# Kernel optimization log

Measured on AMD Instinct MI355X. Metric: run time of the kernel, lower is better.

## Reference

```python
import jax, jax.numpy as jnp
import numpy as np

ND, ED, HD, L, K = 128, 64, 256, 4, 24   # node_dim, edge_dim(num_rbf), hidden_dim, num_layers, max_neighbors
CUTOFF = 8.0
N = 2048  # n_atoms


def _silu(x):
    return x * jax.nn.sigmoid(x)


def _lattice(lengths, angles):
    a, b, c = lengths[0], lengths[1], lengths[2]
    deg = jnp.asarray(np.pi / 180.0, lengths.dtype)
    al, be, ga = angles[0] * deg, angles[1] * deg, angles[2] * deg
    lx = a
    xy = b * jnp.cos(ga)
    xz = c * jnp.cos(be)
    ly = b * jnp.sin(ga)
    yz = (b * c * jnp.cos(al) - xy * xz) / ly
    lz = jnp.sqrt(c ** 2 - xz ** 2 - yz ** 2)
    z = jnp.zeros((), lengths.dtype)
    return jnp.stack([jnp.stack([lx, z, z]), jnp.stack([xy, ly, z]), jnp.stack([xz, yz, lz])])


def _rbf(d):
    centers = jnp.linspace(0.0, CUTOFF, ED)
    widths = jnp.full((ED,), CUTOFF / ED)
    d = d[..., None]
    g = jnp.exp(-(d - centers) ** 2 / (2.0 * widths ** 2))
    cv = 0.5 * (jnp.cos(d * jnp.pi / CUTOFF) + 1.0) * (d < CUTOFF).astype(d.dtype)
    return g * cv


def _forward(atom_types, frac_coords, lengths, angles, timesteps, emb, tW, tb,
             eW1, eb1, eW2, eb2, nW1, nb1, nW2, nb2, cW1, cb1, cW2, cb2):
    n = frac_coords.shape[0]
    lattice = _lattice(lengths, angles)            # [3,3]
    cart = frac_coords @ lattice                   # [n,3]

    # ---- vectorized periodic neighbor graph (replaces host triple loop) ----
    shifts = jnp.asarray(np.array([[i, j, k] for i in (-1, 0, 1) for j in (-1, 0, 1) for k in (-1, 0, 1)],
                                  dtype=np.float32))
    sv = shifts @ lattice                          # [27,3]
    p = cart[None, :, :] + sv[:, None, :]          # [27,n,3] shifted atom positions
    # squared distances without materializing [27,n,n,3]
    d2 = (p * p).sum(-1)[:, :, None] + (cart * cart).sum(-1)[None, None, :] \
         - 2.0 * jnp.einsum('snk,mk->snm', p, cart)      # [27, n_j, n_i]
    dist = jnp.sqrt(jnp.maximum(d2, 1e-12))
    cand = jnp.where((dist < CUTOFF) & (dist > 0.01), dist, jnp.inf)
    cand = cand.reshape(27 * n, n).T               # [n_i, 27*n_j]; flat f = s*n + j
    _, idx = jax.lax.top_k(-cand, K)               # K smallest distances per atom i
    d_k = jnp.take_along_axis(cand, idx, axis=1)   # [n,K]
    dst = (idx % n).reshape(-1)                    # neighbor atom j (edge_list = [i, j])
    src = jnp.repeat(jnp.arange(n), K)             # center atom i
    valid = jnp.isfinite(d_k).reshape(-1)
    m = valid.astype(jnp.float32)[:, None]         # [E,1] pad mask
    d_e = jnp.where(valid, d_k.reshape(-1), 0.0)
    edge_attr = _rbf(d_e)                          # [E, ED]

    # ---- EGNN stack ----
    nf = emb[atom_types] + timesteps @ tW + tb     # [n, ND]
    coords = cart
    seg = lambda x, i: jax.ops.segment_sum(x, i, num_segments=n)
    for l in range(L):
        ef = jnp.concatenate([nf[src], nf[dst], edge_attr], axis=-1)   # [E, 2*ND+ED]
        msg = _silu(_silu(ef @ eW1[l] + eb1[l]) @ eW2[l] + eb2[l])     # [E, HD]
        aggr = seg(msg * m, dst)                                       # [n, HD]
        nf = nf + _silu(jnp.concatenate([nf, aggr], axis=-1) @ nW1[l] + nb1[l]) @ nW2[l] + nb2[l]
        w = _silu(msg @ cW1[l] + cb1[l]) @ cW2[l] + cb2[l]             # [E,1]
        cd = coords[src] - coords[dst]
        cd = cd / (jnp.linalg.norm(cd, axis=-1, keepdims=True) + 1e-8)
        coords = coords + seg(w * cd * m, dst)
    return nf, coords


def setup_inputs() -> dict:
    key = jax.random.key(0)
    ks = jax.random.split(key, 16)
    pr = lambda k, shape: jax.random.normal(k, shape, jnp.float32) * 0.02
    return dict(
        atom_types=jax.random.randint(ks[0], (N,), 0, 100),
        frac_coords=jax.random.uniform(ks[1], (N, 3), jnp.float32),
        lengths=jnp.ones((3,), jnp.float32) * 12.0,
        angles=jnp.ones((3,), jnp.float32) * 90.0,
        timesteps=jax.random.normal(ks[2], (N, 128), jnp.float32),
        emb=pr(ks[3], (100, ND)),
        tW=pr(ks[4], (128, ND)), tb=jnp.zeros((ND,), jnp.float32),
        eW1=pr(ks[5], (L, 2 * ND + ED, HD)), eb1=jnp.zeros((L, HD), jnp.float32),
        eW2=pr(ks[6], (L, HD, HD)), eb2=jnp.zeros((L, HD), jnp.float32),
        nW1=pr(ks[7], (L, ND + HD, HD)), nb1=jnp.zeros((L, HD), jnp.float32),
        nW2=pr(ks[8], (L, HD, ND)), nb2=jnp.zeros((L, ND), jnp.float32),
        cW1=pr(ks[9], (L, HD, HD // 2)), cb1=jnp.zeros((L, HD // 2), jnp.float32),
        cW2=pr(ks[10], (L, HD // 2, 1)), cb2=jnp.zeros((L, 1), jnp.float32),
    )


def reference(atom_types, frac_coords, lengths, angles, timesteps, emb, tW, tb,
              eW1, eb1, eW2, eb2, nW1, nb1, nW2, nb2, cW1, cb1, cW2, cb2):
    return _forward(atom_types, frac_coords, lengths, angles, timesteps, emb, tW, tb,
                    eW1, eb1, eW2, eb2, nW1, nb1, nW2, nb2, cW1, cb1, cW2, cb2)
```

## Files before the change

kernel.cpp:

```cpp
#include <hip/hip_runtime.h>
#include <hip/hip_bf16.h>
#include <math.h>

#define NA 2048
#define KN 24
#define NE (NA*KN)
#define NDIM 128
#define EDIM 64
#define HDIM 256
#define NLAYER 4
#define MAXDEG 256
#define EB 64

typedef __attribute__((ext_vector_type(8))) short bf16x8;
typedef __attribute__((ext_vector_type(4))) float f32x4;

__device__ __forceinline__ float siluf(float x) {
    return __fdividef(x, 1.0f + __expf(-x));
}
__device__ __forceinline__ ushort f2b(float x) {
    __hip_bfloat16 h = __float2bfloat16(x);
    return *reinterpret_cast<ushort*>(&h);
}
__device__ __forceinline__ float b2f(ushort h) { return __uint_as_float(((unsigned)h) << 16); }

__device__ __forceinline__ void gl_lds(const void* g, void* lds) {
    __builtin_amdgcn_global_load_lds(
        (const __attribute__((address_space(1))) unsigned int*)g,
        (__attribute__((address_space(3))) unsigned int*)lds, 16, 0, 0);
}

struct Lat { float lx, xy, xz, ly, yz, lz; };

__device__ __forceinline__ Lat make_lattice(const float* lengths, const float* angles) {
    const float deg = 0.017453292519943295f;
    float a = lengths[0], b = lengths[1], c = lengths[2];
    float al = angles[0]*deg, be = angles[1]*deg, ga = angles[2]*deg;
    Lat L;
    L.lx = a;
    L.xy = b * cosf(ga);
    L.xz = c * cosf(be);
    L.ly = b * sinf(ga);
    L.yz = (b*c*cosf(al) - L.xy*L.xz) / L.ly;
    L.lz = sqrtf(c*c - L.xz*L.xz - L.yz*L.yz);
    return L;
}

__global__ void setup_kernel(const float* __restrict__ frac, const float* __restrict__ lengths,
                             const float* __restrict__ angles, float* __restrict__ cart,
                             float* __restrict__ cxg, float* __restrict__ cyg,
                             float* __restrict__ czg, float* __restrict__ sv,
                             int* __restrict__ ccnt) {
    int i = blockIdx.x*blockDim.x + threadIdx.x;
    Lat L = make_lattice(lengths, angles);
    if (i < NA) {
        float f0 = frac[i*3], f1 = frac[i*3+1], f2 = frac[i*3+2];
        float x = f0*L.lx + f1*L.xy + f2*L.xz;
        float y = f1*L.ly + f2*L.yz;
        float z = f2*L.lz;
        cart[i*3+0] = x; cart[i*3+1] = y; cart[i*3+2] = z;
        cxg[i] = x; cyg[i] = y; czg[i] = z;
        ccnt[i] = 0;
    }
    if (i < 27) {
        float s0 = (float)(i/9 - 1), s1 = (float)((i/3)%3 - 1), s2 = (float)(i%3 - 1);
        sv[i*3+0] = s0*L.lx + s1*L.xy + s2*L.xz;
        sv[i*3+1] = s1*L.ly + s2*L.yz;
        sv[i*3+2] = s2*L.lz;
    }
}

__global__ __launch_bounds__(64) void knn_kernel(
        const float* __restrict__ cxg, const float* __restrict__ cyg,
        const float* __restrict__ czg, const float* __restrict__ lengths,
        const float* __restrict__ angles, const float* __restrict__ sv,
        int* __restrict__ dstl, ushort* __restrict__ rbf16,
        int* __restrict__ ccnt, int* __restrict__ cedg) {
    __shared__ float sd2L[16][64];
    __shared__ int   sfL[16][64];
    const int lane = threadIdx.x;
    const int i = blockIdx.x;
    Lat L = make_lattice(lengths, angles);
    const float deg = 0.017453292519943295f;
    const bool ortho = fabsf(cosf(angles[0]*deg)) < 1e-6f &&
                       fabsf(cosf(angles[1]*deg)) < 1e-6f &&
                       fabsf(cosf(angles[2]*deg)) < 1e-6f;
    const float cx = cxg[i], cy = cyg[i], cz = czg[i];
    const float invlx = 1.0f/L.lx, invly = 1.0f/L.ly, invlz = 1.0f/L.lz;
    float R = 2.8f;
    int mycnt = 0, cnt = 0;
    bool flatm = false;
    for (int attempt = 0; attempt < 8; ++attempt) {
        const float R2 = R*R;
        mycnt = 0;
        flatm = !ortho || (attempt == 7);
        if (!flatm) {
#pragma unroll 2
            for (int j0 = 0; j0 < NA; j0 += 64) {
                const int j = j0 + lane;
                const float dx = cxg[j] - cx, dy = cyg[j] - cy, dz = czg[j] - cz;
                const float kx = rintf(dx*invlx), ky = rintf(dy*invly), kz = rintf(dz*invlz);
                const float ex = dx - (kx*L.lx + ky*L.xy + kz*L.xz);
                const float ey = dy - (ky*L.ly + kz*L.yz);
                const float ez = dz - kz*L.lz;
                const float d2 = fmaf(ex,ex,fmaf(ey,ey,ez*ez));
                if (d2 < R2 && d2 > 1e-4f) {
                    const int s = (1-(int)kx)*9 + (1-(int)ky)*3 + (1-(int)kz);
                    if (mycnt < 16) { sd2L[mycnt][lane] = d2; sfL[mycnt][lane] = (s<<11) + j; }
                    ++mycnt;
                }
            }
            if (__ballot(mycnt > 16)) {
                flatm = true;
            } else {
                int tot = mycnt;
                for (int off = 32; off > 0; off >>= 1) tot += __shfl_xor(tot, off, 64);
                cnt = tot;
            }
        }
        if (flatm) {
            cnt = 0;
            for (int s = 0; s < 27; ++s) {
                const float svx = sv[s*3], svy = sv[s*3+1], svz = sv[s*3+2];
                for (int j0 = 0; j0 < NA; j0 += 64) {
                    const int j = j0 + lane;
                    const float ex = cxg[j] + svx - cx;
                    const float ey = cyg[j] + svy - cy;
                    const float ez = czg[j] + svz - cz;
                    const float d2 = fmaf(ex,ex,fmaf(ey,ey,ez*ez));
                    const bool hit = (d2 < R2) && (d2 > 1e-4f);
                    const unsigned long long m = __ballot(hit);
                    const int rank = __popcll(m & ((1ull<<lane)-1ull));
                    const int slot = cnt + rank;
                    if (hit && slot < 1024) { sd2L[slot>>6][slot&63] = d2; sfL[slot>>6][slot&63] = (s<<11)+j; }
                    cnt += __popcll(m);
                }
            }
            cnt = min(cnt, 1024);
        }
        if (cnt >= KN) break;
        R = fminf(R*1.6f, flatm ? 8.0f : 5.9f);
    }
    int vq;
    if (flatm) vq = (lane < cnt) ? min(16, ((cnt - 1 - lane) >> 6) + 1) : 0;
    else       vq = mycnt;
    unsigned long long key[16];
#pragma unroll
    for (int q = 0; q < 16; ++q) {
        const float d2v = sd2L[q][lane];
        const int fl = sfL[q][lane];
        const unsigned long long kk = ((unsigned long long)__float_as_uint(d2v) << 20)
                                    | ((unsigned long long)(unsigned)fl << 4) | (unsigned)q;
        key[q] = (q < vq) ? kk : ~0ull;
    }
    float der[KN];
    for (int k = 0; k < KN; ++k) {
        unsigned long long lm = key[0];
#pragma unroll
        for (int q = 1; q < 16; ++q) lm = key[q] < lm ? key[q] : lm;
        for (int off = 32; off > 0; off >>= 1) {
            unsigned long long o = __shfl_xor(lm, off, 64);
            lm = o < lm ? o : lm;
        }
        der[k] = sqrtf(__uint_as_float((unsigned)(lm >> 20)));
        if (lane == 0) {
            const int jn = (int)((lm >> 4) & 2047u);
            dstl[i*KN + k] = jn;
            const int slot = atomicAdd(&ccnt[jn], 1);
            if (slot < MAXDEG) cedg[(size_t)jn*MAXDEG + slot] = i*KN + k;
        }
#pragma unroll
        for (int q = 0; q < 16; ++q) if (key[q] == lm) key[q] = ~0ull;
    }
    const float center = (8.0f/63.0f) * (float)lane;
    for (int k = 0; k < KN; ++k) {
        const float d = der[k];
        const float diff = d - center;
        const float g = __expf(diff*diff * -32.0f);
        const float cv = 0.5f * (__cosf(d * (float)(M_PI/8.0)) + 1.0f);
        rbf16[(size_t)(i*KN + k)*EDIM + lane] = f2b(g * cv);
    }
}

__global__ void csort_kernel(const int* __restrict__ ccnt, int* __restrict__ cedg) {
    const int j = blockIdx.x*4 + (threadIdx.x >> 6);
    const int lane = threadIdx.x & 63;
    const int cnt = min(ccnt[j], MAXDEG);
    if (cnt <= 64) {
        int v = (lane < cnt) ? cedg[(size_t)j*MAXDEG + lane] : 0x7FFFFFFF;
#pragma unroll
        for (int k = 2; k <= 64; k <<= 1) {
#pragma unroll
            for (int s = k >> 1; s > 0; s >>= 1) {
                int o = __shfl_xor(v, s, 64);
                const bool up = ((lane & k) == 0);
                const bool lowhalf = ((lane & s) == 0);
                v = ((lowhalf == up) ? min(v, o) : max(v, o));
            }
        }
        if (lane < cnt) cedg[(size_t)j*MAXDEG + lane] = v;
    } else if (lane == 0) {
        int* L = cedg + (size_t)j*MAXDEG;
        for (int a = 1; a < cnt; ++a) {
            int v = L[a]; int b = a - 1;
            while (b >= 0 && L[b] > v) { L[b+1] = L[b]; --b; }
            L[b+1] = v;
        }
    }
}

__global__ void nf_init_kernel(const int* __restrict__ atom_types, const float* __restrict__ ts,
                               const float* __restrict__ emb, const float* __restrict__ tW,
                               const float* __restrict__ tb, float* __restrict__ nf,
                               ushort* __restrict__ nf16) {
    int i = blockIdx.x, c = threadIdx.x;
    float acc = emb[atom_types[i]*NDIM + c] + tb[c];
    for (int kk = 0; kk < 128; ++kk) acc += ts[i*128 + kk] * tW[kk*NDIM + c];
    nf[i*NDIM + c] = acc;
    nf16[i*NDIM + c] = f2b(acc);
}

__global__ void wprep_all(const float* __restrict__ eW1, const float* __restrict__ eW2,
                          const float* __restrict__ cW1, const float* __restrict__ nW1,
                          const float* __restrict__ nW2,
                          ushort* __restrict__ eW1t, ushort* __restrict__ eW2t,
                          ushort* __restrict__ cW1t, ushort* __restrict__ nW1t,
                          ushort* __restrict__ nW2t) {
    __shared__ float tile[64][65];
    const int b = blockIdx.x;
    const float* W; ushort* Wt; int Kk, Nn, rel;
    if (b < 80)       { W = eW1; Wt = eW1t; Kk = 320; Nn = 256; rel = b; }
    else if (b < 144) { W = eW2; Wt = eW2t; Kk = 256; Nn = 256; rel = b - 80; }
    else if (b < 176) { W = cW1; Wt = cW1t; Kk = 256; Nn = 128; rel = b - 144; }
    else if (b < 272) { W = nW1; Wt = nW1t; Kk = 384; Nn = 256; rel = b - 176; }
    else              { W = nW2; Wt = nW2t; Kk = 256; Nn = 128; rel = b - 272; }
    const int kt = Kk >> 6, nt = Nn >> 6, per = kt*nt;
    const int l = rel / per, r2 = rel - l*per;
    const int k0 = (r2 / nt) * 64, n0 = (r2 - (r2/nt)*nt) * 64;
    const float* Wl = W + (size_t)l*Kk*Nn;
    ushort* Wtl = Wt + (size_t)l*Kk*Nn;
    const int tr = threadIdx.x >> 6, tc = threadIdx.x & 63;
#pragma unroll
    for (int q = 0; q < 16; ++q) {
        const int k = q*4 + tr;
        tile[k][tc] = Wl[(size_t)(k0 + k)*Nn + n0 + tc];
    }
    __syncthreads();
#pragma unroll
    for (int q = 0; q < 16; ++q) {
        const int n = q*4 + tr;
        Wtl[(size_t)(n0 + n)*Kk + k0 + tc] = f2b(tile[tc][n]);
    }
}

__global__ __launch_bounds__(256) void edge_fused(
        const ushort* __restrict__ nf16, const int* __restrict__ dstl,
        const ushort* __restrict__ rbf16,
        const ushort* __restrict__ eW1t,
        const ushort* __restrict__ eW2t,
        const ushort* __restrict__ cW1t,
        const float* __restrict__ eb1, const float* __restrict__ eb2,
        const float* __restrict__ cb1, const float* __restrict__ cW2v,
        const float* __restrict__ cb2v,
        ushort* __restrict__ msg16, float* __restrict__ wvout) {
    __shared__ alignas(16) char R0[40960];
    __shared__ alignas(16) char R1[32768];
    __shared__ int sdst[64];
    __shared__ float wred[2][64];
    ushort* As = (ushort*)R0;
    ushort* Bs = (ushort*)(R0 + 8192);
    ushort* B2 = (ushort*)R1;
    ushort* Cs = (ushort*)R1;

    const int t = threadIdx.x, wave = t >> 6, lane = t & 63;
    const int row0 = blockIdx.x*EB;
    if (t < EB) sdst[t] = dstl[row0 + t];
    __syncthreads();
    const int wr = (wave >> 1)*32;
    const int wcB = (wave & 1)*128;
    const int lr = lane & 15, g0 = lane >> 4;

    const int rA_  = wave*16 + (lane >> 2);
    const int gA_  = (lane & 3) ^ ((rA_ >> 1) & 3);
    const int eA_  = row0 + rA_;
    const ushort* baseSrc = nf16  + (size_t)(eA_/KN)*NDIM + gA_*8;
    const ushort* baseDst = nf16  + (size_t)sdst[rA_]*NDIM + gA_*8;
    const ushort* baseRbf = rbf16 + (size_t)eA_*EDIM + gA_*8;
    const uint ldsA_ = (uint)(wave*16)*32;
    const ushort* baseW1[4]; const ushort* baseW2[4];
    uint ldsBq[4];
#pragma unroll
    for (int q = 0; q < 4; ++q) {
        const int rowb = wave*64 + q*16 + (lane >> 2);
        const int gB = (lane & 3) ^ ((rowb >> 1) & 3);
        baseW1[q] = eW1t + (size_t)rowb*320 + gB*8;
        baseW2[q] = eW2t + (size_t)rowb*256 + gB*8;
        ldsBq[q] = (uint)(wave*64 + q*16)*32;
    }
    const ushort* baseC[2];
    uint ldsCq[2];
#pragma unroll
    for (int q = 0; q < 2; ++q) {
        const int rowb = wave*32 + q*16 + (lane >> 2);
        const int gB = (lane & 3) ^ ((rowb >> 1) & 3);
        baseC[q] = cW1t + (size_t)rowb*256 + gB*8;
        ldsCq[q] = (uint)(wave*32 + q*16)*32;
    }

    auto STAGEA = [&](int buf, int k0) {
        const ushort* gp = (k0 < NDIM) ? baseSrc + k0
                         : (k0 < 2*NDIM) ? baseDst + (k0 - NDIM)
                         : baseRbf + (k0 - 2*NDIM);
        gl_lds(gp, As + (size_t)buf*2048 + ldsA_);
#pragma unroll
        for (int q = 0; q < 4; ++q)
            gl_lds(baseW1[q] + k0, Bs + (size_t)buf*8192 + ldsBq[q]);
    };
    f32x4 acc[2][8];
#pragma unroll
    for (int m = 0; m < 2; ++m)
#pragma unroll
        for (int n = 0; n < 8; ++n) acc[m][n] = (f32x4){0.f,0.f,0.f,0.f};
    STAGEA(0, 0);
    int cur = 0;
#pragma unroll
    for (int it = 0; it < 10; ++it) {
        if (it + 1 < 10) {
            STAGEA(cur ^ 1, (it + 1)*32);
            asm volatile("s_waitcnt vmcnt(5)" ::: "memory");
        } else {
            asm volatile("s_waitcnt vmcnt(0)" ::: "memory");
        }
        __builtin_amdgcn_s_barrier();
        bf16x8 af[2], bfr[8];
#pragma unroll
        for (int m = 0; m < 2; ++m) {
            const int rA = wr + m*16 + lr;
            af[m] = *reinterpret_cast<const bf16x8*>(&As[cur*2048 + rA*32 + ((g0 ^ ((rA>>1)&3)))*8]);
        }
#pragma unroll
        for (int n = 0; n < 8; ++n) {
            const int rB = wcB + n*16 + lr;
            bfr[n] = *reinterpret_cast<const bf16x8*>(&Bs[(size_t)cur*8192 + rB*32 + ((g0 ^ ((rB>>1)&3)))*8]);
        }
        __builtin_amdgcn_s_setprio(1);
#pragma unroll
        for (int m = 0; m < 2; ++m)
#pragma unroll
            for (int n = 0; n < 8; ++n)
                acc[m][n] = __builtin_amdgcn_mfma_f32_16x16x32_bf16(af[m], bfr[n], acc[m][n], 0, 0, 0);
        __builtin_amdgcn_s_setprio(0);
        __builtin_amdgcn_s_barrier();
        cur ^= 1;
    }
    {
#pragma unroll
        for (int q = 0; q < 4; ++q)
            gl_lds(baseW2[q], B2 + ldsBq[q]);
    }
#pragma unroll
    for (int n = 0; n < 8; ++n) {
        const int cc = wcB + n*16 + lr;
        const float b1 = eb1[cc];
#pragma unroll
        for (int m = 0; m < 2; ++m) {
#pragma unroll
            for (int j = 0; j < 4; ++j) {
                const int rr = wr + m*16 + g0*4 + j;
                const float x = siluf(acc[m][n][j] + b1);
                *(ushort*)(R0 + rr*512 + ((cc*2) ^ ((rr&7)<<4))) = f2b(x);
            }
        }
    }
    __syncthreads();

#pragma unroll
    for (int m = 0; m < 2; ++m)
#pragma unroll
        for (int n = 0; n < 8; ++n) acc[m][n] = (f32x4){0.f,0.f,0.f,0.f};
    cur = 0;
#pragma unroll
    for (int it = 0; it < 8; ++it) {
        if (it + 1 < 8) {
            const int k0 = (it + 1)*32;
#pragma unroll
            for (int q = 0; q < 4; ++q)
                gl_lds(baseW2[q] + k0, B2 + (size_t)(cur^1)*8192 + ldsBq[q]);
            asm volatile("s_waitcnt vmcnt(4)" ::: "memory");
        } else {
            asm volatile("s_waitcnt vmcnt(0)" ::: "memory");
        }
        __builtin_amdgcn_s_barrier();
        bf16x8 af[2], bfr[8];
#pragma unroll
        for (int m = 0; m < 2; ++m) {
            const int rA = wr + m*16 + lr;
            const int kc = it*4 + g0;
            af[m] = *reinterpret_cast<const bf16x8*>(R0 + rA*512 + ((kc*16) ^ ((rA&7)<<4)));
        }
#pragma unroll
        for (int n = 0; n < 8; ++n) {
            const int rB = wcB + n*16 + lr;
            bfr[n] = *reinterpret_cast<const bf16x8*>(&B2[(size_t)cur*8192 + rB*32 + ((g0 ^ ((rB>>1)&3)))*8]);
        }
        __builtin_amdgcn_s_setprio(1);
#pragma unroll
        for (int m = 0; m < 2; ++m)
#pragma unroll
            for (int n = 0; n < 8; ++n)
                acc[m][n] = __builtin_amdgcn_mfma_f32_16x16x32_bf16(af[m], bfr[n], acc[m][n], 0, 0, 0);
        __builtin_amdgcn_s_setprio(0);
        __builtin_amdgcn_s_barrier();
        cur ^= 1;
    }
    {
#pragma unroll
        for (int q = 0; q < 2; ++q)
            gl_lds(baseC[q], Cs + ldsCq[q]);
    }
#pragma unroll
    for (int n = 0; n < 8; ++n) {
        const int cc = wcB + n*16 + lr;
        const float b2 = eb2[cc];
#pragma unroll
        for (int m = 0; m < 2; ++m) {
#pragma unroll
            for (int j = 0; j < 4; ++j) {
                const int rr = wr + m*16 + g0*4 + j;
                *(ushort*)(R0 + rr*512 + ((cc*2) ^ ((rr&7)<<4))) = f2b(siluf(acc[m][n][j] + b2));
            }
        }
    }
    __syncthreads();

    const int wcC = (wave & 1)*64;
    f32x4 acc3[2][4];
#pragma unroll
    for (int m = 0; m < 2; ++m)
#pragma unroll
        for (int n = 0; n < 4; ++n) acc3[m][n] = (f32x4){0.f,0.f,0.f,0.f};
    cur = 0;
#pragma unroll
    for (int it = 0; it < 8; ++it) {
        if (it + 1 < 8) {
            const int k0 = (it + 1)*32;
#pragma unroll
            for (int q = 0; q < 2; ++q)
                gl_lds(baseC[q] + k0, Cs + (size_t)(cur^1)*4096 + ldsCq[q]);
            asm volatile("s_waitcnt vmcnt(2)" ::: "memory");
        } else {
            asm volatile("s_waitcnt vmcnt(0)" ::: "memory");
        }
        __builtin_amdgcn_s_barrier();
        bf16x8 af[2], bfr[4];
#pragma unroll
        for (int m = 0; m < 2; ++m) {
            const int rA = wr + m*16 + lr;
            const int kc = it*4 + g0;
            af[m] = *reinterpret_cast<const bf16x8*>(R0 + rA*512 + ((kc*16) ^ ((rA&7)<<4)));
        }
#pragma unroll
        for (int n = 0; n < 4; ++n) {
            const int rB = wcC + n*16 + lr;
            bfr[n] = *reinterpret_cast<const bf16x8*>(&Cs[(size_t)cur*4096 + rB*32 + ((g0 ^ ((rB>>1)&3)))*8]);
        }
        __builtin_amdgcn_s_setprio(1);
#pragma unroll
        for (int m = 0; m < 2; ++m)
#pragma unroll
            for (int n = 0; n < 4; ++n)
                acc3[m][n] = __builtin_amdgcn_mfma_f32_16x16x32_bf16(af[m], bfr[n], acc3[m][n], 0, 0, 0);
        __builtin_amdgcn_s_setprio(0);
        __builtin_amdgcn_s_barrier();
        cur ^= 1;
    }
    float part[2][4];
#pragma unroll
    for (int m = 0; m < 2; ++m)
#pragma unroll
        for (int j = 0; j < 4; ++j) part[m][j] = 0.0f;
#pragma unroll
    for (int n = 0; n < 4; ++n) {
        const int cc = wcC + n*16 + lr;
        const float bb = cb1[cc];
        const float cw = cW2v[cc];
#pragma unroll
        for (int m = 0; m < 2; ++m)
#pragma unroll
            for (int j = 0; j < 4; ++j)
                part[m][j] += siluf(acc3[m][n][j] + bb) * cw;
    }
#pragma unroll
    for (int off = 1; off < 16; off <<= 1)
#pragma unroll
        for (int m = 0; m < 2; ++m)
#pragma unroll
            for (int j = 0; j < 4; ++j)
                part[m][j] += __shfl_xor(part[m][j], off, 64);
    if (lr == 0) {
#pragma unroll
        for (int m = 0; m < 2; ++m)
#pragma unroll
            for (int j = 0; j < 4; ++j)
                wred[wave & 1][wr + m*16 + g0*4 + j] = part[m][j];
    }
    __syncthreads();
    if (t < EB) wvout[row0 + t] = wred[0][t] + wred[1][t] + cb2v[0];
#pragma unroll
    for (int k = 0; k < 8; ++k) {
        const int off = (t + k*256) * 16;
        const int row = off >> 9;
        const int cg = ((off >> 4) & 31) ^ (row & 7);
        uint4 v = *reinterpret_cast<const uint4*>(R0 + off);
        *reinterpret_cast<uint4*>(msg16 + (size_t)(row0 + row)*256 + cg*8) = v;
    }
}

__global__ __launch_bounds__(256) void nodefused(
        const ushort* __restrict__ nf16, const ushort* __restrict__ aggr16,
        const ushort* __restrict__ nW1t,
        const ushort* __restrict__ nW2t,
        const float* __restrict__ nb1, const float* __restrict__ nb2,
        float* __restrict__ nf, ushort* __restrict__ nf16out) {
    __shared__ alignas(16) ushort Ab[12*2048];
    __shared__ alignas(16) char HsB[32768];
    __shared__ alignas(16) ushort Bs[2][256*32];
    const int t = threadIdx.x, wave = t >> 6, lane = t & 63;
    const int r0 = blockIdx.x*64;
    const int wr = (wave >> 1)*32;
    const int wcB = (wave & 1)*128;
    const int lr = lane & 15, g0 = lane >> 4;

#pragma unroll
    for (int c = 0; c < 3; ++c) {
        const int ks = wave*3 + c;
#pragma unroll
        for (int q = 0; q < 4; ++q) {
            const int r = q*16 + (lane >> 2);
            const int g = (lane & 3) ^ ((r >> 1) & 3);
            const int col = ks*32 + g*8;
            const ushort* gp = (col < NDIM)
                ? nf16 + (size_t)(r0 + r)*NDIM + col
                : aggr16 + (size_t)(r0 + r)*HDIM + (col - NDIM);
            gl_lds(gp, Ab + ks*2048 + q*16*32);
        }
    }
    const ushort* baseW1[4];
    uint ldsBq[4];
#pragma unroll
    for (int q = 0; q < 4; ++q) {
        const int rowb = wave*64 + q*16 + (lane >> 2);
        const int gB = (lane & 3) ^ ((rowb >> 1) & 3);
        baseW1[q] = nW1t + (size_t)rowb*384 + gB*8;
        ldsBq[q] = (uint)(wave*64 + q*16)*32;
    }
    const ushort* baseW2[2];
    uint ldsCq[2];
#pragma unroll
    for (int q = 0; q < 2; ++q) {
        const int rowb = wave*32 + q*16 + (lane >> 2);
        const int gB = (lane & 3) ^ ((rowb >> 1) & 3);
        baseW2[q] = nW2t + (size_t)rowb*256 + gB*8;
        ldsCq[q] = (uint)(wave*32 + q*16)*32;
    }
#pragma unroll
    for (int q = 0; q < 4; ++q)
        gl_lds(baseW1[q], &Bs[0][ldsBq[q]]);
    asm volatile("s_waitcnt vmcnt(0)" ::: "memory");
    __builtin_amdgcn_s_barrier();

    f32x4 acc[2][8];
#pragma unroll
    for (int m = 0; m < 2; ++m)
#pragma unroll
        for (int n = 0; n < 8; ++n) acc[m][n] = (f32x4){0.f,0.f,0.f,0.f};
    int cur = 0;
#pragma unroll
    for (int it = 0; it < 12; ++it) {
        if (it + 1 < 12) {
            const int k0 = (it + 1)*32;
#pragma unroll
            for (int q = 0; q < 4; ++q)
                gl_lds(baseW1[q] + k0, &Bs[cur^1][ldsBq[q]]);
            asm volatile("s_waitcnt vmcnt(4)" ::: "memory");
        } else {
            asm volatile("s_waitcnt vmcnt(0)" ::: "memory");
        }
        __builtin_amdgcn_s_barrier();
        bf16x8 af[2], bfr[8];
#pragma unroll
        for (int m = 0; m < 2; ++m) {
            const int rA = wr + m*16 + lr;
            af[m] = *reinterpret_cast<const bf16x8*>(&Ab[it*2048 + rA*32 + ((g0 ^ ((rA>>1)&3)))*8]);
        }
#pragma unroll
        for (int n = 0; n < 8; ++n) {
            const int rB = wcB + n*16 + lr;
            bfr[n] = *reinterpret_cast<const bf16x8*>(&Bs[cur][rB*32 + ((g0 ^ ((rB>>1)&3)))*8]);
        }
        __builtin_amdgcn_s_setprio(1);
#pragma unroll
        for (int m = 0; m < 2; ++m)
#pragma unroll
            for (int n = 0; n < 8; ++n)
                acc[m][n] = __builtin_amdgcn_mfma_f32_16x16x32_bf16(af[m], bfr[n], acc[m][n], 0, 0, 0);
        __builtin_amdgcn_s_setprio(0);
        __builtin_amdgcn_s_barrier();
        cur ^= 1;
    }
#pragma unroll
    for (int q = 0; q < 2; ++q)
        gl_lds(baseW2[q], &Bs[0][ldsCq[q]]);
#pragma unroll
    for (int n = 0; n < 8; ++n) {
        const int cc = wcB + n*16 + lr;
        const float b1 = nb1[cc];
#pragma unroll
        for (int m = 0; m < 2; ++m) {
#pragma unroll
            for (int j = 0; j < 4; ++j) {
                const int rr = wr + m*16 + g0*4 + j;
                *(ushort*)(HsB + rr*512 + ((cc*2) ^ ((rr&7)<<4))) = f2b(siluf(acc[m][n][j] + b1));
            }
        }
    }
    __syncthreads();

    const int wcC = (wave & 1)*64;
    f32x4 acc3[2][4];
#pragma unroll
    for (int m = 0; m < 2; ++m)
#pragma unroll
        for (int n = 0; n < 4; ++n) acc3[m][n] = (f32x4){0.f,0.f,0.f,0.f};
    cur = 0;
#pragma unroll
    for (int it = 0; it < 8; ++it) {
        if (it + 1 < 8) {
            const int k0 = (it + 1)*32;
#pragma unroll
            for (int q = 0; q < 2; ++q)
                gl_lds(baseW2[q] + k0, &Bs[cur^1][ldsCq[q]]);
            asm volatile("s_waitcnt vmcnt(2)" ::: "memory");
        } else {
            asm volatile("s_waitcnt vmcnt(0)" ::: "memory");
        }
        __builtin_amdgcn_s_barrier();
        bf16x8 af[2], bfr[4];
#pragma unroll
        for (int m = 0; m < 2; ++m) {
            const int rA = wr + m*16 + lr;
            const int kc = it*4 + g0;
            af[m] = *reinterpret_cast<const bf16x8*>(HsB + rA*512 + ((kc*16) ^ ((rA&7)<<4)));
        }
#pragma unroll
        for (int n = 0; n < 4; ++n) {
            const int rB = wcC + n*16 + lr;
            bfr[n] = *reinterpret_cast<const bf16x8*>(&Bs[cur][rB*32 + ((g0 ^ ((rB>>1)&3)))*8]);
        }
        __builtin_amdgcn_s_setprio(1);
#pragma unroll
        for (int m = 0; m < 2; ++m)
#pragma unroll
            for (int n = 0; n < 4; ++n)
                acc3[m][n] = __builtin_amdgcn_mfma_f32_16x16x32_bf16(af[m], bfr[n], acc3[m][n], 0, 0, 0);
        __builtin_amdgcn_s_setprio(0);
        __builtin_amdgcn_s_barrier();
        cur ^= 1;
    }
#pragma unroll
    for (int n = 0; n < 4; ++n) {
        const int cc = wcC + n*16 + lr;
        const float b2 = nb2[cc];
#pragma unroll
        for (int m = 0; m < 2; ++m) {
#pragma unroll
            for (int j = 0; j < 4; ++j) {
                const int rr = r0 + wr + m*16 + g0*4 + j;
                float x = acc3[m][n][j] + b2 + nf[(size_t)rr*NDIM + cc];
                nf[(size_t)rr*NDIM + cc] = x;
                nf16out[(size_t)rr*NDIM + cc] = f2b(x);
            }
        }
    }
}

__global__ void node_kernel(const ushort* __restrict__ msg16, const float* __restrict__ cold,
                            const float* __restrict__ wv, const int* __restrict__ ccnt,
                            const int* __restrict__ cedg,
                            ushort* __restrict__ aggr16, float* __restrict__ cnew) {
    __shared__ int se[4][64];
    const int w = threadIdx.x >> 6, lane = threadIdx.x & 63;
    const int j = blockIdx.x*4 + w;
    const int cnt = min(ccnt[j], MAXDEG);
    se[w][lane] = (lane < cnt) ? cedg[(size_t)j*MAXDEG + lane] : 0;
    __syncthreads();
    const int c4 = lane*4;
    float s0 = 0, s1 = 0, s2 = 0, s3 = 0;
    const int lim = min(cnt, 64);
    for (int q = 0; q < lim; ++q) {
        const int e = se[w][q];
        ushort4 v = *reinterpret_cast<const ushort4*>(&msg16[(size_t)e*HDIM + c4]);
        s0 += b2f(v.x); s1 += b2f(v.y); s2 += b2f(v.z); s3 += b2f(v.w);
    }
    for (int q = 64; q < cnt; ++q) {
        const int e = cedg[(size_t)j*MAXDEG + q];
        ushort4 v = *reinterpret_cast<const ushort4*>(&msg16[(size_t)e*HDIM + c4]);
        s0 += b2f(v.x); s1 += b2f(v.y); s2 += b2f(v.z); s3 += b2f(v.w);
    }
    ushort4 o; o.x = f2b(s0); o.y = f2b(s1); o.z = f2b(s2); o.w = f2b(s3);
    *reinterpret_cast<ushort4*>(&aggr16[(size_t)j*HDIM + c4]) = o;
    const float jx = cold[j*3], jy = cold[j*3+1], jz = cold[j*3+2];
    float dx = 0, dy = 0, dz = 0;
    for (int q = lane; q < cnt; q += 64) {
        const int e = (q < 64) ? se[w][q] : cedg[(size_t)j*MAXDEG + q];
        const int si = e / KN;
        const float ax = cold[si*3]   - jx;
        const float ay = cold[si*3+1] - jy;
        const float az = cold[si*3+2] - jz;
        const float inv = wv[e] / (sqrtf(ax*ax + ay*ay + az*az) + 1e-8f);
        dx += inv*ax; dy += inv*ay; dz += inv*az;
    }
    for (int off = 32; off > 0; off >>= 1) {
        dx += __shfl_xor(dx, off, 64);
        dy += __shfl_xor(dy, off, 64);
        dz += __shfl_xor(dz, off, 64);
    }
    if (lane == 0) {
        cnew[j*3]   = jx + dx;
        cnew[j*3+1] = jy + dy;
        cnew[j*3+2] = jz + dz;
    }
}

__global__ void copyout_kernel(const float* __restrict__ nf, const float* __restrict__ coords,
                               float* __restrict__ out) {
    int idx = blockIdx.x*256 + threadIdx.x;
    if (idx < NA*NDIM) out[idx] = nf[idx];
    else if (idx < NA*NDIM + NA*3) out[idx] = coords[idx - NA*NDIM];
}

extern "C" void kernel_launch(void* const* d_in, const int* in_sizes, int n_in,
                              void* d_out, int out_size, void* d_ws, size_t ws_size,
                              hipStream_t stream) {
    const int*   atom_types = (const int*)  d_in[0];
    const float* frac       = (const float*)d_in[1];
    const float* lengths    = (const float*)d_in[2];
    const float* angles     = (const float*)d_in[3];
    const float* timesteps  = (const float*)d_in[4];
    const float* emb        = (const float*)d_in[5];
    const float* tW         = (const float*)d_in[6];
    const float* tb         = (const float*)d_in[7];
    const float* eW1        = (const float*)d_in[8];
    const float* eb1        = (const float*)d_in[9];
    const float* eW2        = (const float*)d_in[10];
    const float* eb2        = (const float*)d_in[11];
    const float* nW1        = (const float*)d_in[12];
    const float* nb1        = (const float*)d_in[13];
    const float* nW2        = (const float*)d_in[14];
    const float* nb2        = (const float*)d_in[15];
    const float* cW1        = (const float*)d_in[16];
    const float* cb1        = (const float*)d_in[17];
    const float* cW2        = (const float*)d_in[18];
    const float* cb2        = (const float*)d_in[19];

    char* p = (char*)d_ws;
    auto alloc = [&](size_t bytes) { char* q = p; p += (bytes + 255) & ~(size_t)255; return q; };
    float*  sv    = (float*) alloc(81*4);
    float*  c0    = (float*) alloc((size_t)NA*3*4);
    float*  c1    = (float*) alloc((size_t)NA*3*4);
    float*  cxg   = (float*) alloc((size_t)NA*4);
    float*  cyg   = (float*) alloc((size_t)NA*4);
    float*  czg   = (float*) alloc((size_t)NA*4);
    float*  nf    = (float*) alloc((size_t)NA*NDIM*4);
    int*    dstl  = (int*)   alloc((size_t)NE*4);
    ushort* rbf16 = (ushort*)alloc((size_t)NE*EDIM*2);
    int*    ccnt  = (int*)   alloc((size_t)NA*4);
    int*    cedg  = (int*)   alloc((size_t)NA*MAXDEG*4);
    ushort* aggr16= (ushort*)alloc((size_t)NA*HDIM*2);
    float*  wv    = (float*) alloc((size_t)NE*4);
    ushort* nf16  = (ushort*)alloc((size_t)NA*NDIM*2);
    ushort* msg16 = (ushort*)alloc((size_t)NE*HDIM*2);
    ushort* eW1t  = (ushort*)alloc((size_t)NLAYER*(2*NDIM+EDIM)*HDIM*2);
    ushort* eW2t  = (ushort*)alloc((size_t)NLAYER*HDIM*HDIM*2);
    ushort* cW1t  = (ushort*)alloc((size_t)NLAYER*(HDIM/2)*HDIM*2);
    ushort* nW1t  = (ushort*)alloc((size_t)NLAYER*(NDIM+HDIM)*HDIM*2);
    ushort* nW2t  = (ushort*)alloc((size_t)NLAYER*HDIM*NDIM*2);

    setup_kernel<<<8, 256, 0, stream>>>(frac, lengths, angles, c0, cxg, cyg, czg, sv, ccnt);
    knn_kernel<<<NA, 64, 0, stream>>>(cxg, cyg, czg, lengths, angles, sv,
                                      dstl, rbf16, ccnt, cedg);
    csort_kernel<<<NA/4, 256, 0, stream>>>(ccnt, cedg);
    nf_init_kernel<<<NA, 128, 0, stream>>>(atom_types, timesteps, emb, tW, tb, nf, nf16);
    wprep_all<<<304, 256, 0, stream>>>(eW1, eW2, cW1, nW1, nW2,
                                       eW1t, eW2t, cW1t, nW1t, nW2t);

    float* cin = c0; float* cout = c1;
    for (int l = 0; l < NLAYER; ++l) {
        const float* eb1l = eb1 + (size_t)l*HDIM;
        const float* eb2l = eb2 + (size_t)l*HDIM;
        const float* nb1l = nb1 + (size_t)l*HDIM;
        const float* nb2l = nb2 + (size_t)l*NDIM;
        const float* cb1l = cb1 + (size_t)l*(HDIM/2);
        const float* cW2l = cW2 + (size_t)l*(HDIM/2);
        const float* cb2l = cb2 + (size_t)l;

        edge_fused<<<NE/EB, 256, 0, stream>>>(
            nf16, dstl, rbf16,
            eW1t + (size_t)l*(2*NDIM+EDIM)*HDIM, eW2t + (size_t)l*HDIM*HDIM,
            cW1t + (size_t)l*(HDIM/2)*HDIM,
            eb1l, eb2l, cb1l, cW2l, cb2l, msg16, wv);
        node_kernel<<<NA/4, 256, 0, stream>>>(msg16, cin, wv, ccnt, cedg, aggr16, cout);
        nodefused<<<NA/64, 256, 0, stream>>>(
            nf16, aggr16, nW1t + (size_t)l*(NDIM+HDIM)*HDIM, nW2t + (size_t)l*HDIM*NDIM,
            nb1l, nb2l, nf, nf16);
        float* tmp = cin; cin = cout; cout = tmp;
    }
    copyout_kernel<<<(NA*NDIM + NA*3)/256, 256, 0, stream>>>(nf, cin, (float*)d_out);
}
```

Baseline: 363.0 us.

## Enlarge edge-kernel tile to 96 rows and single-buffer second and third GEMM weights

```diff
diff --git a/kernel.cpp b/kernel.cpp
--- a/kernel.cpp
+++ b/kernel.cpp
@@ -10,7 +10,7 @@
 #define HDIM 256
 #define NLAYER 4
 #define MAXDEG 256
-#define EB 64
+#define EB 96
 
 typedef __attribute__((ext_vector_type(8))) short bf16x8;
 typedef __attribute__((ext_vector_type(4))) float f32x4;
@@ -263,12 +263,12 @@
         const float* __restrict__ cb1, const float* __restrict__ cW2v,
         const float* __restrict__ cb2v,
         ushort* __restrict__ msg16, float* __restrict__ wvout) {
-    __shared__ alignas(16) char R0[40960];
-    __shared__ alignas(16) char R1[32768];
-    __shared__ int sdst[64];
-    __shared__ float wred[2][64];
+    __shared__ alignas(16) char R0[49152];
+    __shared__ alignas(16) char R1[16384];
+    __shared__ int sdst[96];
+    __shared__ float wred[2][96];
     ushort* As = (ushort*)R0;
-    ushort* Bs = (ushort*)(R0 + 8192);
+    ushort* Bs = (ushort*)(R0 + 12288);
     ushort* B2 = (ushort*)R1;
     ushort* Cs = (ushort*)R1;
 
@@ -276,17 +276,10 @@
     const int row0 = blockIdx.x*EB;
     if (t < EB) sdst[t] = dstl[row0 + t];
     __syncthreads();
-    const int wr = (wave >> 1)*32;
+    const int wr = (wave >> 1)*48;
     const int wcB = (wave & 1)*128;
     const int lr = lane & 15, g0 = lane >> 4;
 
-    const int rA_  = wave*16 + (lane >> 2);
-    const int gA_  = (lane & 3) ^ ((rA_ >> 1) & 3);
-    const int eA_  = row0 + rA_;
-    const ushort* baseSrc = nf16  + (size_t)(eA_/KN)*NDIM + gA_*8;
-    const ushort* baseDst = nf16  + (size_t)sdst[rA_]*NDIM + gA_*8;
-    const ushort* baseRbf = rbf16 + (size_t)eA_*EDIM + gA_*8;
-    const uint ldsA_ = (uint)(wave*16)*32;
     const ushort* baseW1[4]; const ushort* baseW2[4];
     uint ldsBq[4];
 #pragma unroll
@@ -308,17 +301,27 @@
     }
 
     auto STAGEA = [&](int buf, int k0) {
-        const ushort* gp = (k0 < NDIM) ? baseSrc + k0
-                         : (k0 < 2*NDIM) ? baseDst + (k0 - NDIM)
-                         : baseRbf + (k0 - 2*NDIM);
-        gl_lds(gp, As + (size_t)buf*2048 + ldsA_);
+        const int na = (wave < 2) ? 2 : 1;
+        const int a0 = (wave < 2) ? wave*2 : wave + 2;
+        for (int q = 0; q < na; ++q) {
+            const int grp = a0 + q;
+            const int r = grp*16 + (lane >> 2);
+            const int g = (lane & 3) ^ ((r >> 1) & 3);
+            const int kg = k0 + g*8;
+            const int e = row0 + r;
+            const ushort* gp;
+            if (kg < NDIM)        gp = nf16 + (size_t)(e/KN)*NDIM + kg;
+            else if (kg < 2*NDIM) gp = nf16 + (size_t)sdst[r]*NDIM + (kg - NDIM);
+            else                  gp = rbf16 + (size_t)e*EDIM + (kg - 2*NDIM);
+            gl_lds(gp, As + (size_t)buf*3072 + grp*512);
+        }
 #pragma unroll
         for (int q = 0; q < 4; ++q)
             gl_lds(baseW1[q] + k0, Bs + (size_t)buf*8192 + ldsBq[q]);
     };
-    f32x4 acc[2][8];
-#pragma unroll
-    for (int m = 0; m < 2; ++m)
+    f32x4 acc[3][8];
+#pragma unroll
+    for (int m = 0; m < 3; ++m)
 #pragma unroll
         for (int n = 0; n < 8; ++n) acc[m][n] = (f32x4){0.f,0.f,0.f,0.f};
     STAGEA(0, 0);
@@ -327,16 +330,17 @@
     for (int it = 0; it < 10; ++it) {
         if (it + 1 < 10) {
             STAGEA(cur ^ 1, (it + 1)*32);
-            asm volatile("s_waitcnt vmcnt(5)" ::: "memory");
+            if (wave < 2) asm volatile("s_waitcnt vmcnt(6)" ::: "memory");
+            else          asm volatile("s_waitcnt vmcnt(5)" ::: "memory");
         } else {
             asm volatile("s_waitcnt vmcnt(0)" ::: "memory");
         }
         __builtin_amdgcn_s_barrier();
-        bf16x8 af[2], bfr[8];
-#pragma unroll
-        for (int m = 0; m < 2; ++m) {
+        bf16x8 af[3], bfr[8];
+#pragma unroll
+        for (int m = 0; m < 3; ++m) {
             const int rA = wr + m*16 + lr;
-            af[m] = *reinterpret_cast<const bf16x8*>(&As[cur*2048 + rA*32 + ((g0 ^ ((rA>>1)&3)))*8]);
+            af[m] = *reinterpret_cast<const bf16x8*>(&As[cur*3072 + rA*32 + ((g0 ^ ((rA>>1)&3)))*8]);
         }
 #pragma unroll
         for (int n = 0; n < 8; ++n) {
@@ -345,7 +349,7 @@
         }
         __builtin_amdgcn_s_setprio(1);
 #pragma unroll
-        for (int m = 0; m < 2; ++m)
+        for (int m = 0; m < 3; ++m)
 #pragma unroll
             for (int n = 0; n < 8; ++n)
                 acc[m][n] = __builtin_amdgcn_mfma_f32_16x16x32_bf16(af[m], bfr[n], acc[m][n], 0, 0, 0);
@@ -363,7 +367,7 @@
         const int cc = wcB + n*16 + lr;
         const float b1 = eb1[cc];
 #pragma unroll
-        for (int m = 0; m < 2; ++m) {
+        for (int m = 0; m < 3; ++m) {
 #pragma unroll
             for (int j = 0; j < 4; ++j) {
                 const int rr = wr + m*16 + g0*4 + j;
@@ -375,25 +379,16 @@
     __syncthreads();
 
 #pragma unroll
-    for (int m = 0; m < 2; ++m)
+    for (int m = 0; m < 3; ++m)
 #pragma unroll
         for (int n = 0; n < 8; ++n) acc[m][n] = (f32x4){0.f,0.f,0.f,0.f};
-    cur = 0;
 #pragma unroll
     for (int it = 0; it < 8; ++it) {
-        if (it + 1 < 8) {
-            const int k0 = (it + 1)*32;
-#pragma unroll
-            for (int q = 0; q < 4; ++q)
-                gl_lds(baseW2[q] + k0, B2 + (size_t)(cur^1)*8192 + ldsBq[q]);
-            asm volatile("s_waitcnt vmcnt(4)" ::: "memory");
-        } else {
-            asm volatile("s_waitcnt vmcnt(0)" ::: "memory");
-        }
-        __builtin_amdgcn_s_barrier();
-        bf16x8 af[2], bfr[8];
-#pragma unroll
-        for (int m = 0; m < 2; ++m) {
+        asm volatile("s_waitcnt vmcnt(0)" ::: "memory");
+        __builtin_amdgcn_s_barrier();
+        bf16x8 af[3], bfr[8];
+#pragma unroll
+        for (int m = 0; m < 3; ++m) {
             const int rA = wr + m*16 + lr;
             const int kc = it*4 + g0;
             af[m] = *reinterpret_cast<const bf16x8*>(R0 + rA*512 + ((kc*16) ^ ((rA&7)<<4)));
@@ -401,17 +396,22 @@
 #pragma unroll
         for (int n = 0; n < 8; ++n) {
             const int rB = wcB + n*16 + lr;
-            bfr[n] = *reinterpret_cast<const bf16x8*>(&B2[(size_t)cur*8192 + rB*32 + ((g0 ^ ((rB>>1)&3)))*8]);
+            bfr[n] = *reinterpret_cast<const bf16x8*>(&B2[rB*32 + ((g0 ^ ((rB>>1)&3)))*8]);
         }
         __builtin_amdgcn_s_setprio(1);
 #pragma unroll
-        for (int m = 0; m < 2; ++m)
+        for (int m = 0; m < 3; ++m)
 #pragma unroll
             for (int n = 0; n < 8; ++n)
                 acc[m][n] = __builtin_amdgcn_mfma_f32_16x16x32_bf16(af[m], bfr[n], acc[m][n], 0, 0, 0);
         __builtin_amdgcn_s_setprio(0);
         __builtin_amdgcn_s_barrier();
-        cur ^= 1;
+        if (it + 1 < 8) {
+            const int k0 = (it + 1)*32;
+#pragma unroll
+            for (int q = 0; q < 4; ++q)
+                gl_lds(baseW2[q] + k0, B2 + ldsBq[q]);
+        }
     }
     {
 #pragma unroll
@@ -423,7 +423,7 @@
         const int cc = wcB + n*16 + lr;
         const float b2 = eb2[cc];
 #pragma unroll
-        for (int m = 0; m < 2; ++m) {
+        for (int m = 0; m < 3; ++m) {
 #pragma unroll
             for (int j = 0; j < 4; ++j) {
                 const int rr = wr + m*16 + g0*4 + j;
@@ -434,27 +434,18 @@
     __syncthreads();
 
     const int wcC = (wave & 1)*64;
-    f32x4 acc3[2][4];
-#pragma unroll
-    for (int m = 0; m < 2; ++m)
+    f32x4 acc3[3][4];
+#pragma unroll
+    for (int m = 0; m < 3; ++m)
 #pragma unroll
         for (int n = 0; n < 4; ++n) acc3[m][n] = (f32x4){0.f,0.f,0.f,0.f};
-    cur = 0;
 #pragma unroll
     for (int it = 0; it < 8; ++it) {
-        if (it + 1 < 8) {
-            const int k0 = (it + 1)*32;
-#pragma unroll
-            for (int q = 0; q < 2; ++q)
-                gl_lds(baseC[q] + k0, Cs + (size_t)(cur^1)*4096 + ldsCq[q]);
-            asm volatile("s_waitcnt vmcnt(2)" ::: "memory");
-        } else {
-            asm volatile("s_waitcnt vmcnt(0)" ::: "memory");
-        }
-        __builtin_amdgcn_s_barrier();
-        bf16x8 af[2], bfr[4];
-#pragma unroll
-        for (int m = 0; m < 2; ++m) {
+        asm volatile("s_waitcnt vmcnt(0)" ::: "memory");
+        __builtin_amdgcn_s_barrier();
+        bf16x8 af[3], bfr[4];
+#pragma unroll
+        for (int m = 0; m < 3; ++m) {
             const int rA = wr + m*16 + lr;
             const int kc = it*4 + g0;
             af[m] = *reinterpret_cast<const bf16x8*>(R0 + rA*512 + ((kc*16) ^ ((rA&7)<<4)));
@@ -462,21 +453,26 @@
 #pragma unroll
         for (int n = 0; n < 4; ++n) {
             const int rB = wcC + n*16 + lr;
-            bfr[n] = *reinterpret_cast<const bf16x8*>(&Cs[(size_t)cur*4096 + rB*32 + ((g0 ^ ((rB>>1)&3)))*8]);
+            bfr[n] = *reinterpret_cast<const bf16x8*>(&Cs[rB*32 + ((g0 ^ ((rB>>1)&3)))*8]);
         }
         __builtin_amdgcn_s_setprio(1);
 #pragma unroll
-        for (int m = 0; m < 2; ++m)
+        for (int m = 0; m < 3; ++m)
 #pragma unroll
             for (int n = 0; n < 4; ++n)
                 acc3[m][n] = __builtin_amdgcn_mfma_f32_16x16x32_bf16(af[m], bfr[n], acc3[m][n], 0, 0, 0);
         __builtin_amdgcn_s_setprio(0);
         __builtin_amdgcn_s_barrier();
-        cur ^= 1;
-    }
-    float part[2][4];
-#pragma unroll
-    for (int m = 0; m < 2; ++m)
+        if (it + 1 < 8) {
+            const int k0 = (it + 1)*32;
+#pragma unroll
+            for (int q = 0; q < 2; ++q)
+                gl_lds(baseC[q] + k0, Cs + ldsCq[q]);
+        }
+    }
+    float part[3][4];
+#pragma unroll
+    for (int m = 0; m < 3; ++m)
 #pragma unroll
         for (int j = 0; j < 4; ++j) part[m][j] = 0.0f;
 #pragma unroll
@@ -485,7 +481,7 @@
         const float bb = cb1[cc];
         const float cw = cW2v[cc];
 #pragma unroll
-        for (int m = 0; m < 2; ++m)
+        for (int m = 0; m < 3; ++m)
 #pragma unroll
             for (int j = 0; j < 4; ++j)
                 part[m][j] += siluf(acc3[m][n][j] + bb) * cw;
@@ -493,13 +489,13 @@
 #pragma unroll
     for (int off = 1; off < 16; off <<= 1)
 #pragma unroll
-        for (int m = 0; m < 2; ++m)
+        for (int m = 0; m < 3; ++m)
 #pragma unroll
             for (int j = 0; j < 4; ++j)
                 part[m][j] += __shfl_xor(part[m][j], off, 64);
     if (lr == 0) {
 #pragma unroll
-        for (int m = 0; m < 2; ++m)
+        for (int m = 0; m < 3; ++m)
 #pragma unroll
             for (int j = 0; j < 4; ++j)
                 wred[wave & 1][wr + m*16 + g0*4 + j] = part[m][j];
@@ -507,7 +503,7 @@
     __syncthreads();
     if (t < EB) wvout[row0 + t] = wred[0][t] + wred[1][t] + cb2v[0];
 #pragma unroll
-    for (int k = 0; k < 8; ++k) {
+    for (int k = 0; k < 12; ++k) {
         const int off = (t + k*256) * 16;
         const int row = off >> 9;
         const int cg = ((off >> 4) & 31) ^ (row & 7);
```

Measured after the change: 404.4 us. +11.4%, slower.
